# Performance work log

Measured on AMD Instinct MI355X. Metric: run time of the kernel, lower is better.

Reference implementation:

```python
import jax, jax.numpy as jnp
import numpy as np

N_NODES = 50000
N_EDGES = 800000
F_IN = 256
HEADS = 8
OUT_CH = 10  # hard-coded in the source GATv2Conv(in, 10, heads=H)
HIDDEN = HEADS * OUT_CH  # 80
NEG_SLOPE = 0.2  # PyG GATv2Conv default


def _gatv2_layer(x, src, dst, Wl, Wr, att, b, n):
    """One GATv2Conv layer (eval mode, concat=True, self-loops already added).
    x: [n, F_in]; src/dst: [E_tot] int; Wl/Wr: [F_in, H*C]; att: [H, C]; b: [H*C].
    """
    xl = (x @ Wl).reshape(n, HEADS, OUT_CH)  # source-side transform
    xr = (x @ Wr).reshape(n, HEADS, OUT_CH)  # target-side transform
    # gather -> LeakyReLU -> attention logit per edge/head
    e = jax.nn.leaky_relu(xl[src] + xr[dst], NEG_SLOPE)      # [E, H, C]
    logits = jnp.einsum('ehc,hc->eh', e, att)                # [E, H]
    # segment softmax over incoming edges of each target node
    m = jax.ops.segment_max(logits, dst, num_segments=n)     # [n, H]
    ex = jnp.exp(logits - m[dst])
    denom = jax.ops.segment_sum(ex, dst, num_segments=n)     # [n, H]
    alpha = ex / (denom[dst] + 1e-16)                        # [E, H]
    # scatter-add aggregation of weighted source messages
    out = jax.ops.segment_sum(xl[src] * alpha[:, :, None], dst, num_segments=n)
    return out.reshape(n, HIDDEN) + b


def _gat_forward(x, edge_index, params):
    n = x.shape[0]
    loops = jnp.arange(n, dtype=edge_index.dtype)
    src = jnp.concatenate([edge_index[0], loops])  # add self loops (PyG default)
    dst = jnp.concatenate([edge_index[1], loops])
    for (Wl, Wr, att, b) in params:
        x = jax.nn.elu(_gatv2_layer(x, src, dst, Wl, Wr, att, b, n))
    return x


def setup_inputs() -> dict:
    key = jax.random.key(0)
    ks = jax.random.split(key, 16)
    x = jax.random.normal(ks[0], (N_NODES, F_IN), dtype=jnp.float32)
    edge_index = jax.random.randint(ks[1], (2, N_EDGES), 0, N_NODES, dtype=jnp.int64)
    inp = {'x': x, 'edge_index': edge_index}
    dims_in = [F_IN, HIDDEN, HIDDEN]
    for i, d_in in enumerate(dims_in):
        k0, k1, k2 = jax.random.split(ks[2 + i], 3)
        s = 1.0 / np.sqrt(d_in)
        inp[f'Wl{i}'] = jax.random.normal(k0, (d_in, HIDDEN), dtype=jnp.float32) * s
        inp[f'Wr{i}'] = jax.random.normal(k1, (d_in, HIDDEN), dtype=jnp.float32) * s
        inp[f'att{i}'] = jax.random.normal(k2, (HEADS, OUT_CH), dtype=jnp.float32) * 0.1
        inp[f'b{i}'] = jnp.zeros((HIDDEN,), dtype=jnp.float32)
    return inp


def reference(x, edge_index, Wl0, Wr0, att0, b0, Wl1, Wr1, att1, b1, Wl2, Wr2, att2, b2):
    params = [(Wl0, Wr0, att0, b0), (Wl1, Wr1, att1, b1), (Wl2, Wr2, att2, b2)]
    return _gat_forward(x, edge_index, params)
```

## Files before the change

kernel.cpp:

```cpp
#include <hip/hip_runtime.h>
#include <math.h>

#define N_NODES 50000
#define N_EDGES 800000
#define E_TOT   (N_EDGES + N_NODES)
#define HEADS   8
#define OUTC    10
#define HID     80
#define NEG_SLOPE 0.2f


__global__ __launch_bounds__(256) void hist_k(const int* __restrict__ ei, int* __restrict__ cnt) {
    int e = blockIdx.x * blockDim.x + threadIdx.x;
    if (e >= E_TOT) return;
    int d = (e < N_EDGES) ? ei[N_EDGES + e] : (e - N_EDGES);
    atomicAdd(&cnt[d], 1);
}

__global__ __launch_bounds__(1024) void scan_k(const int* __restrict__ cnt, int* __restrict__ rowptr) {
    __shared__ int wsum[16];
    __shared__ int carry_s;
    const int tid = threadIdx.x;
    const int lane = tid & 63, wid = tid >> 6;
    if (tid == 0) carry_s = 0;
    __syncthreads();
    for (int base = 0; base < N_NODES; base += 1024) {
        int i = base + tid;
        int v = (i < N_NODES) ? cnt[i] : 0;
        int s = v;
        #pragma unroll
        for (int off = 1; off < 64; off <<= 1) {
            int t = __shfl_up(s, off, 64);
            if (lane >= off) s += t;
        }
        if (lane == 63) wsum[wid] = s;
        int carry = carry_s;
        __syncthreads();
        if (wid == 0 && lane < 16) {
            int w = wsum[lane];
            #pragma unroll
            for (int off = 1; off < 16; off <<= 1) {
                int t = __shfl_up(w, off, 16);
                if (lane >= off) w += t;
            }
            wsum[lane] = w;
        }
        __syncthreads();
        int woff = (wid > 0) ? wsum[wid - 1] : 0;
        int incl = s + woff;
        int excl = incl - v;
        if (i < N_NODES) rowptr[i] = carry + excl;
        int total = wsum[15];
        __syncthreads();
        if (tid == 0) carry_s = carry + total;
        __syncthreads();
    }
    if (tid == 0) rowptr[N_NODES] = carry_s;
}

__global__ __launch_bounds__(256) void scatter_k(const int* __restrict__ ei,
                                                 const int* __restrict__ rowptr,
                                                 int* __restrict__ cursor,
                                                 int* __restrict__ csr) {
    int e = blockIdx.x * blockDim.x + threadIdx.x;
    if (e >= E_TOT) return;
    int s, d;
    if (e < N_EDGES) { s = ei[e]; d = ei[N_EDGES + e]; }
    else { s = e - N_EDGES; d = s; }
    int pos = rowptr[d] + atomicAdd(&cursor[d], 1);
    csr[pos] = s;
}


__global__ __launch_bounds__(256) void gemm3_k(const float* __restrict__ A, int K,
                                               const float* __restrict__ Wl,
                                               const float* __restrict__ Wr,
                                               float* __restrict__ xl,
                                               float* __restrict__ xr) {
    __shared__ float4 sa[64][4];
    const int tid = threadIdx.x;
    const int lane = tid & 63;
    const int wv = __builtin_amdgcn_readfirstlane(tid >> 6);
    const int mat = wv >> 1;
    const int j0 = (wv & 1) * 40;
    const int row0 = blockIdx.x * 64;
    const int row = row0 + lane;

    const float* __restrict__ W = mat ? Wr : Wl;
    float* __restrict__ Xo = mat ? xr : xl;

    const int lr = tid >> 2;
    const int lq = tid & 3;
    const int lrow = (row0 + lr < N_NODES) ? (row0 + lr) : (N_NODES - 1);
    const float* __restrict__ Asrc = A + (size_t)lrow * K + lq * 4;

    float acc[40];
    #pragma unroll
    for (int j = 0; j < 40; ++j) acc[j] = 0.f;

    for (int kb = 0; kb < K; kb += 16) {
        sa[lr][lq] = *reinterpret_cast<const float4*>(Asrc + kb);
        __syncthreads();

        float4 ar[4];
        #pragma unroll
        for (int q = 0; q < 4; ++q) ar[q] = sa[lane][q];

        #pragma unroll
        for (int q = 0; q < 4; ++q) {
            #pragma unroll
            for (int t = 0; t < 4; ++t) {
                const float av = (t == 0) ? ar[q].x : (t == 1) ? ar[q].y
                               : (t == 2) ? ar[q].z : ar[q].w;
                const float* __restrict__ wrow = W + (size_t)(kb + q * 4 + t) * HID + j0;
                #pragma unroll
                for (int c4 = 0; c4 < 10; ++c4) {
                    const float4 w = *reinterpret_cast<const float4*>(wrow + c4 * 4);
                    acc[c4 * 4 + 0] = fmaf(av, w.x, acc[c4 * 4 + 0]);
                    acc[c4 * 4 + 1] = fmaf(av, w.y, acc[c4 * 4 + 1]);
                    acc[c4 * 4 + 2] = fmaf(av, w.z, acc[c4 * 4 + 2]);
                    acc[c4 * 4 + 3] = fmaf(av, w.w, acc[c4 * 4 + 3]);
                }
            }
        }
        __syncthreads();
    }

    if (row < N_NODES) {
        float* op = Xo + (size_t)row * HID + j0;
        #pragma unroll
        for (int c4 = 0; c4 < 10; ++c4)
            *reinterpret_cast<float4*>(op + c4 * 4) =
                make_float4(acc[c4 * 4 + 0], acc[c4 * 4 + 1], acc[c4 * 4 + 2], acc[c4 * 4 + 3]);
    }
}


__global__ __launch_bounds__(256) void agg2_k(const float* __restrict__ xl,
                                              const float* __restrict__ xr,
                                              const int* __restrict__ rowptr,
                                              const int* __restrict__ csr,
                                              const float* __restrict__ att,
                                              const float* __restrict__ bias,
                                              float* __restrict__ out) {
    const int tid = threadIdx.x;
    const int lane = tid & 63;
    const int node = blockIdx.x * 4 + (tid >> 6);
    if (node >= N_NODES) return;
    const int eg = lane >> 3;
    const int h = lane & 7;
    const int cb = h * 10;

    float att10[10], xr10[10];
    #pragma unroll
    for (int c = 0; c < 10; ++c) {
        att10[c] = att[cb + c];
        xr10[c] = xr[(size_t)node * HID + cb + c];
    }
    const int ro = rowptr[node];
    const int deg = rowptr[node + 1] - ro;

    float m = -INFINITY, s = 0.f;
    float acc[10];
    #pragma unroll
    for (int c = 0; c < 10; ++c) acc[c] = 0.f;

    for (int i = eg; i < deg; i += 8) {
        const int src = csr[ro + i];
        const float* xlp = xl + (size_t)src * HID + cb;
        float xl10[10];
        float logit = 0.f;
        #pragma unroll
        for (int c = 0; c < 10; ++c) {
            xl10[c] = xlp[c];
            float e = xl10[c] + xr10[c];
            e = (e > 0.f) ? e : NEG_SLOPE * e;
            logit = fmaf(e, att10[c], logit);
        }
        const float nm = fmaxf(m, logit);
        const float scale = __expf(m - nm);
        const float p = __expf(logit - nm);
        s = s * scale + p;
        #pragma unroll
        for (int c = 0; c < 10; ++c) acc[c] = acc[c] * scale + p * xl10[c];
        m = nm;
    }

    #pragma unroll
    for (int off = 8; off <= 32; off <<= 1) {
        const float om = __shfl_xor(m, off, 64);
        const float os = __shfl_xor(s, off, 64);
        float oacc[10];
        #pragma unroll
        for (int c = 0; c < 10; ++c) oacc[c] = __shfl_xor(acc[c], off, 64);
        const float nm = fmaxf(m, om);
        const float sc1 = (m == -INFINITY) ? 0.f : __expf(m - nm);
        const float sc2 = (om == -INFINITY) ? 0.f : __expf(om - nm);
        s = s * sc1 + os * sc2;
        #pragma unroll
        for (int c = 0; c < 10; ++c) acc[c] = acc[c] * sc1 + oacc[c] * sc2;
        m = nm;
    }

    if (lane < 8) {
        const float inv = 1.f / (s + 1e-16f);
        #pragma unroll
        for (int c = 0; c < 10; ++c) {
            float v = acc[c] * inv + bias[cb + c];
            v = (v > 0.f) ? v : (__expf(v) - 1.f);
            out[(size_t)node * HID + cb + c] = v;
        }
    }
}


extern "C" void kernel_launch(void* const* d_in, const int* in_sizes, int n_in,
                              void* d_out, int out_size, void* d_ws, size_t ws_size,
                              hipStream_t stream) {
    const float* x  = (const float*)d_in[0];
    const int*   ei = (const int*)d_in[1];
    const float* Wl[3]   = {(const float*)d_in[2], (const float*)d_in[6],  (const float*)d_in[10]};
    const float* Wr[3]   = {(const float*)d_in[3], (const float*)d_in[7],  (const float*)d_in[11]};
    const float* attp[3] = {(const float*)d_in[4], (const float*)d_in[8],  (const float*)d_in[12]};
    const float* bp[3]   = {(const float*)d_in[5], (const float*)d_in[9],  (const float*)d_in[13]};

    char* ws = (char*)d_ws;
    size_t off = 0;
    auto alloc = [&](size_t bytes) -> void* {
        void* p = ws + off;
        off += (bytes + 255) & ~(size_t)255;
        return p;
    };
    int* cnt    = (int*)alloc((size_t)N_NODES * 4);
    int* cursor = (int*)alloc((size_t)N_NODES * 4);
    int* rowptr = (int*)alloc((size_t)(N_NODES + 1) * 4);
    int* csr    = (int*)alloc((size_t)E_TOT * 4);
    float* xl   = (float*)alloc((size_t)N_NODES * HID * 4);
    float* xr   = (float*)alloc((size_t)N_NODES * HID * 4);
    float* actA = (float*)alloc((size_t)N_NODES * HID * 4);
    float* actB = (float*)alloc((size_t)N_NODES * HID * 4);

    hipMemsetAsync(cnt, 0, (size_t)N_NODES * 4, stream);
    hipMemsetAsync(cursor, 0, (size_t)N_NODES * 4, stream);

    hist_k<<<(E_TOT + 255) / 256, 256, 0, stream>>>(ei, cnt);
    scan_k<<<1, 1024, 0, stream>>>(cnt, rowptr);
    scatter_k<<<(E_TOT + 255) / 256, 256, 0, stream>>>(ei, rowptr, cursor, csr);

    for (int l = 0; l < 3; ++l) {
        const float* act_in = (l == 0) ? x : (l == 1 ? actA : actB);
        const int K = (l == 0) ? 256 : 80;
        gemm3_k<<<(N_NODES + 63) / 64, 256, 0, stream>>>(act_in, K, Wl[l], Wr[l], xl, xr);
        float* out_l = (l == 0) ? actA : (l == 1 ? actB : (float*)d_out);
        agg2_k<<<N_NODES / 4, 256, 0, stream>>>(xl, xr, rowptr, csr, attp[l], bp[l], out_l);
    }
}
```

Before: 557.2 us.

## Use transposed activation layout so GEMM reads coalesced columns without LDS

Adds a tiled transpose of the input features and makes the aggregation kernel write its activations in feature-major (transposed) layout for the next layer. The new GEMM kernel reads two adjacent rows per lane directly from global memory, with no shared-memory staging or barriers. Each wave computes 20 output columns, and a grid dimension selects Wl or Wr. The aim is to remove LDS syncs and raise per-thread reuse. In exchange it adds an extra transpose pass, and the transposed stores from aggregation are strided and poorly coalesced.

```diff
diff --git a/kernel.cpp b/kernel.cpp
--- a/kernel.cpp
+++ b/kernel.cpp
@@ -4,6 +4,7 @@
 #define N_NODES 50000
 #define N_EDGES 800000
 #define E_TOT   (N_EDGES + N_NODES)
+#define F_IN    256
 #define HEADS   8
 #define OUTC    10
 #define HID     80
@@ -72,66 +73,86 @@
 }
 
 
-__global__ __launch_bounds__(256) void gemm3_k(const float* __restrict__ A, int K,
+__global__ __launch_bounds__(256) void transp_k(const float* __restrict__ in,
+                                                float* __restrict__ outT) {
+    __shared__ float t[64][65];
+    const int tx = threadIdx.x & 63;
+    const int ty = threadIdx.x >> 6;
+    const int r0 = blockIdx.x * 64;
+    const int c0 = blockIdx.y * 64;
+    #pragma unroll
+    for (int i = 0; i < 16; ++i) {
+        int r = ty * 16 + i;
+        int gr = r0 + r;
+        if (gr < N_NODES) t[r][tx] = in[(size_t)gr * F_IN + c0 + tx];
+    }
+    __syncthreads();
+    #pragma unroll
+    for (int i = 0; i < 16; ++i) {
+        int c = ty * 16 + i;
+        int gr = r0 + tx;
+        if (gr < N_NODES) outT[(size_t)(c0 + c) * N_NODES + gr] = t[tx][c];
+    }
+}
+
+
+__global__ __launch_bounds__(256) void gemm4_k(const float* __restrict__ AT, int K,
                                                const float* __restrict__ Wl,
                                                const float* __restrict__ Wr,
                                                float* __restrict__ xl,
                                                float* __restrict__ xr) {
-    __shared__ float4 sa[64][4];
-    const int tid = threadIdx.x;
-    const int lane = tid & 63;
-    const int wv = __builtin_amdgcn_readfirstlane(tid >> 6);
-    const int mat = wv >> 1;
-    const int j0 = (wv & 1) * 40;
-    const int row0 = blockIdx.x * 64;
-    const int row = row0 + lane;
+    const int lane = threadIdx.x & 63;
+    const int wv = __builtin_amdgcn_readfirstlane(threadIdx.x >> 6);
+    const int mat = blockIdx.y;
+    const int j0 = wv * 20;
+    const int row0 = blockIdx.x * 128;
+    const int rbase = row0 + 2 * lane;
+    const int rload = (rbase <= N_NODES - 2) ? rbase : (N_NODES - 2);
 
     const float* __restrict__ W = mat ? Wr : Wl;
     float* __restrict__ Xo = mat ? xr : xl;
 
-    const int lr = tid >> 2;
-    const int lq = tid & 3;
-    const int lrow = (row0 + lr < N_NODES) ? (row0 + lr) : (N_NODES - 1);
-    const float* __restrict__ Asrc = A + (size_t)lrow * K + lq * 4;
-
-    float acc[40];
-    #pragma unroll
-    for (int j = 0; j < 40; ++j) acc[j] = 0.f;
-
-    for (int kb = 0; kb < K; kb += 16) {
-        sa[lr][lq] = *reinterpret_cast<const float4*>(Asrc + kb);
-        __syncthreads();
-
-        float4 ar[4];
-        #pragma unroll
-        for (int q = 0; q < 4; ++q) ar[q] = sa[lane][q];
-
-        #pragma unroll
-        for (int q = 0; q < 4; ++q) {
+    float acc0[20], acc1[20];
+    #pragma unroll
+    for (int j = 0; j < 20; ++j) { acc0[j] = 0.f; acc1[j] = 0.f; }
+
+    for (int kb = 0; kb < K; kb += 4) {
+        float2 a[4];
+        #pragma unroll
+        for (int t = 0; t < 4; ++t)
+            a[t] = *reinterpret_cast<const float2*>(AT + (size_t)(kb + t) * N_NODES + rload);
+        #pragma unroll
+        for (int t = 0; t < 4; ++t) {
+            const float* __restrict__ wrow = W + (size_t)(kb + t) * HID + j0;
+            const float ax = a[t].x, ay = a[t].y;
             #pragma unroll
-            for (int t = 0; t < 4; ++t) {
-                const float av = (t == 0) ? ar[q].x : (t == 1) ? ar[q].y
-                               : (t == 2) ? ar[q].z : ar[q].w;
-                const float* __restrict__ wrow = W + (size_t)(kb + q * 4 + t) * HID + j0;
-                #pragma unroll
-                for (int c4 = 0; c4 < 10; ++c4) {
-                    const float4 w = *reinterpret_cast<const float4*>(wrow + c4 * 4);
-                    acc[c4 * 4 + 0] = fmaf(av, w.x, acc[c4 * 4 + 0]);
-                    acc[c4 * 4 + 1] = fmaf(av, w.y, acc[c4 * 4 + 1]);
-                    acc[c4 * 4 + 2] = fmaf(av, w.z, acc[c4 * 4 + 2]);
-                    acc[c4 * 4 + 3] = fmaf(av, w.w, acc[c4 * 4 + 3]);
-                }
+            for (int q = 0; q < 5; ++q) {
+                const float4 w = *reinterpret_cast<const float4*>(wrow + q * 4);
+                acc0[q * 4 + 0] = fmaf(ax, w.x, acc0[q * 4 + 0]);
+                acc0[q * 4 + 1] = fmaf(ax, w.y, acc0[q * 4 + 1]);
+                acc0[q * 4 + 2] = fmaf(ax, w.z, acc0[q * 4 + 2]);
+                acc0[q * 4 + 3] = fmaf(ax, w.w, acc0[q * 4 + 3]);
+                acc1[q * 4 + 0] = fmaf(ay, w.x, acc1[q * 4 + 0]);
+                acc1[q * 4 + 1] = fmaf(ay, w.y, acc1[q * 4 + 1]);
+                acc1[q * 4 + 2] = fmaf(ay, w.z, acc1[q * 4 + 2]);
+                acc1[q * 4 + 3] = fmaf(ay, w.w, acc1[q * 4 + 3]);
             }
         }
-        __syncthreads();
-    }
-
-    if (row < N_NODES) {
-        float* op = Xo + (size_t)row * HID + j0;
-        #pragma unroll
-        for (int c4 = 0; c4 < 10; ++c4)
-            *reinterpret_cast<float4*>(op + c4 * 4) =
-                make_float4(acc[c4 * 4 + 0], acc[c4 * 4 + 1], acc[c4 * 4 + 2], acc[c4 * 4 + 3]);
+    }
+
+    if (rbase < N_NODES) {
+        float* op = Xo + (size_t)rbase * HID + j0;
+        #pragma unroll
+        for (int q = 0; q < 5; ++q)
+            *reinterpret_cast<float4*>(op + q * 4) =
+                make_float4(acc0[q * 4 + 0], acc0[q * 4 + 1], acc0[q * 4 + 2], acc0[q * 4 + 3]);
+    }
+    if (rbase + 1 < N_NODES) {
+        float* op = Xo + (size_t)(rbase + 1) * HID + j0;
+        #pragma unroll
+        for (int q = 0; q < 5; ++q)
+            *reinterpret_cast<float4*>(op + q * 4) =
+                make_float4(acc1[q * 4 + 0], acc1[q * 4 + 1], acc1[q * 4 + 2], acc1[q * 4 + 3]);
     }
 }
 
@@ -142,7 +163,8 @@
                                               const int* __restrict__ csr,
                                               const float* __restrict__ att,
                                               const float* __restrict__ bias,
-                                              float* __restrict__ out) {
+                                              float* __restrict__ out,
+                                              float* __restrict__ outT) {
     const int tid = threadIdx.x;
     const int lane = tid & 63;
     const int node = blockIdx.x * 4 + (tid >> 6);
@@ -208,7 +230,8 @@
         for (int c = 0; c < 10; ++c) {
             float v = acc[c] * inv + bias[cb + c];
             v = (v > 0.f) ? v : (__expf(v) - 1.f);
-            out[(size_t)node * HID + cb + c] = v;
+            if (outT) outT[(size_t)(cb + c) * N_NODES + node] = v;
+            else      out[(size_t)node * HID + cb + c] = v;
         }
     }
 }
@@ -237,8 +260,9 @@
     int* csr    = (int*)alloc((size_t)E_TOT * 4);
     float* xl   = (float*)alloc((size_t)N_NODES * HID * 4);
     float* xr   = (float*)alloc((size_t)N_NODES * HID * 4);
-    float* actA = (float*)alloc((size_t)N_NODES * HID * 4);
-    float* actB = (float*)alloc((size_t)N_NODES * HID * 4);
+    float* xT   = (float*)alloc((size_t)F_IN * N_NODES * 4);
+    float* actAT = xT;
+    float* actBT = xT + (size_t)HID * N_NODES;
 
     hipMemsetAsync(cnt, 0, (size_t)N_NODES * 4, stream);
     hipMemsetAsync(cursor, 0, (size_t)N_NODES * 4, stream);
@@ -247,11 +271,16 @@
     scan_k<<<1, 1024, 0, stream>>>(cnt, rowptr);
     scatter_k<<<(E_TOT + 255) / 256, 256, 0, stream>>>(ei, rowptr, cursor, csr);
 
+    transp_k<<<dim3(782, 4), 256, 0, stream>>>(x, xT);
+
+    const float* AT_l[3] = {xT, actAT, actBT};
+    float* outT_l[3]     = {actAT, actBT, nullptr};
     for (int l = 0; l < 3; ++l) {
-        const float* act_in = (l == 0) ? x : (l == 1 ? actA : actB);
-        const int K = (l == 0) ? 256 : 80;
-        gemm3_k<<<(N_NODES + 63) / 64, 256, 0, stream>>>(act_in, K, Wl[l], Wr[l], xl, xr);
-        float* out_l = (l == 0) ? actA : (l == 1 ? actB : (float*)d_out);
-        agg2_k<<<N_NODES / 4, 256, 0, stream>>>(xl, xr, rowptr, csr, attp[l], bp[l], out_l);
-    }
-}
+        const int K = (l == 0) ? F_IN : HID;
+        gemm4_k<<<dim3((N_NODES + 127) / 128, 2), 256, 0, stream>>>(
+            AT_l[l], K, Wl[l], Wr[l], xl, xr);
+        float* out_l = (l == 2) ? (float*)d_out : nullptr;
+        agg2_k<<<N_NODES / 4, 256, 0, stream>>>(xl, xr, rowptr, csr, attp[l], bp[l],
+                                                out_l, outT_l[l]);
+    }
+}
```

Result: slower. 610.3 us (+9.5%).

## Retile node-feature GEMM to 128-row blocks with two rows per thread

Applied to the files above, without the earlier changes.

The dual-weight GEMM is restructured so each block handles 128 rows for one weight matrix, chosen by blockIdx.y. Each wave owns 20 output columns and each thread computes two rows, so every weight float4 load feeds two rows of FMAs. The A tile is stored transposed in shared memory as 16x128 floats. This is meant to halve weight-load traffic per FMA and improve register reuse, at the cost of more blocks and some shared-memory bank conflicts on the transposed stores.

```diff
diff --git a/kernel.cpp b/kernel.cpp
--- a/kernel.cpp
+++ b/kernel.cpp
@@ -4,6 +4,7 @@
 #define N_NODES 50000
 #define N_EDGES 800000
 #define E_TOT   (N_EDGES + N_NODES)
+#define F_IN    256
 #define HEADS   8
 #define OUTC    10
 #define HID     80
@@ -72,66 +73,78 @@
 }
 
 
-__global__ __launch_bounds__(256) void gemm3_k(const float* __restrict__ A, int K,
+__global__ __launch_bounds__(256) void gemm5_k(const float* __restrict__ A, int K,
                                                const float* __restrict__ Wl,
                                                const float* __restrict__ Wr,
                                                float* __restrict__ xl,
                                                float* __restrict__ xr) {
-    __shared__ float4 sa[64][4];
+    __shared__ float sa[16][128];
     const int tid = threadIdx.x;
     const int lane = tid & 63;
     const int wv = __builtin_amdgcn_readfirstlane(tid >> 6);
-    const int mat = wv >> 1;
-    const int j0 = (wv & 1) * 40;
-    const int row0 = blockIdx.x * 64;
-    const int row = row0 + lane;
+    const int mat = blockIdx.y;
+    const int j0 = wv * 20;
+    const int row0 = blockIdx.x * 128;
 
     const float* __restrict__ W = mat ? Wr : Wl;
     float* __restrict__ Xo = mat ? xr : xl;
 
-    const int lr = tid >> 2;
-    const int lq = tid & 3;
-    const int lrow = (row0 + lr < N_NODES) ? (row0 + lr) : (N_NODES - 1);
-    const float* __restrict__ Asrc = A + (size_t)lrow * K + lq * 4;
-
-    float acc[40];
-    #pragma unroll
-    for (int j = 0; j < 40; ++j) acc[j] = 0.f;
+    const int sr = tid >> 2;
+    const int sq = tid & 3;
+
+    float acc0[20], acc1[20];
+    #pragma unroll
+    for (int j = 0; j < 20; ++j) { acc0[j] = 0.f; acc1[j] = 0.f; }
 
     for (int kb = 0; kb < K; kb += 16) {
-        sa[lr][lq] = *reinterpret_cast<const float4*>(Asrc + kb);
-        __syncthreads();
-
-        float4 ar[4];
-        #pragma unroll
-        for (int q = 0; q < 4; ++q) ar[q] = sa[lane][q];
-
-        #pragma unroll
-        for (int q = 0; q < 4; ++q) {
+        #pragma unroll
+        for (int h = 0; h < 2; ++h) {
+            const int gr = row0 + h * 64 + sr;
+            const int grc = (gr < N_NODES) ? gr : (N_NODES - 1);
+            const float4 v = *reinterpret_cast<const float4*>(
+                A + (size_t)grc * K + kb + sq * 4);
+            sa[sq * 4 + 0][h * 64 + sr] = v.x;
+            sa[sq * 4 + 1][h * 64 + sr] = v.y;
+            sa[sq * 4 + 2][h * 64 + sr] = v.z;
+            sa[sq * 4 + 3][h * 64 + sr] = v.w;
+        }
+        __syncthreads();
+        #pragma unroll
+        for (int k = 0; k < 16; ++k) {
+            const float a0 = sa[k][lane];
+            const float a1 = sa[k][64 + lane];
+            const float* __restrict__ wrow = W + (size_t)(kb + k) * HID + j0;
             #pragma unroll
-            for (int t = 0; t < 4; ++t) {
-                const float av = (t == 0) ? ar[q].x : (t == 1) ? ar[q].y
-                               : (t == 2) ? ar[q].z : ar[q].w;
-                const float* __restrict__ wrow = W + (size_t)(kb + q * 4 + t) * HID + j0;
-                #pragma unroll
-                for (int c4 = 0; c4 < 10; ++c4) {
-                    const float4 w = *reinterpret_cast<const float4*>(wrow + c4 * 4);
-                    acc[c4 * 4 + 0] = fmaf(av, w.x, acc[c4 * 4 + 0]);
-                    acc[c4 * 4 + 1] = fmaf(av, w.y, acc[c4 * 4 + 1]);
-                    acc[c4 * 4 + 2] = fmaf(av, w.z, acc[c4 * 4 + 2]);
-                    acc[c4 * 4 + 3] = fmaf(av, w.w, acc[c4 * 4 + 3]);
-                }
+            for (int q = 0; q < 5; ++q) {
+                const float4 w = *reinterpret_cast<const float4*>(wrow + q * 4);
+                acc0[q * 4 + 0] = fmaf(a0, w.x, acc0[q * 4 + 0]);
+                acc0[q * 4 + 1] = fmaf(a0, w.y, acc0[q * 4 + 1]);
+                acc0[q * 4 + 2] = fmaf(a0, w.z, acc0[q * 4 + 2]);
+                acc0[q * 4 + 3] = fmaf(a0, w.w, acc0[q * 4 + 3]);
+                acc1[q * 4 + 0] = fmaf(a1, w.x, acc1[q * 4 + 0]);
+                acc1[q * 4 + 1] = fmaf(a1, w.y, acc1[q * 4 + 1]);
+                acc1[q * 4 + 2] = fmaf(a1, w.z, acc1[q * 4 + 2]);
+                acc1[q * 4 + 3] = fmaf(a1, w.w, acc1[q * 4 + 3]);
             }
         }
         __syncthreads();
     }
 
-    if (row < N_NODES) {
-        float* op = Xo + (size_t)row * HID + j0;
-        #pragma unroll
-        for (int c4 = 0; c4 < 10; ++c4)
-            *reinterpret_cast<float4*>(op + c4 * 4) =
-                make_float4(acc[c4 * 4 + 0], acc[c4 * 4 + 1], acc[c4 * 4 + 2], acc[c4 * 4 + 3]);
+    const int r0 = row0 + lane;
+    if (r0 < N_NODES) {
+        float* op = Xo + (size_t)r0 * HID + j0;
+        #pragma unroll
+        for (int q = 0; q < 5; ++q)
+            *reinterpret_cast<float4*>(op + q * 4) =
+                make_float4(acc0[q * 4 + 0], acc0[q * 4 + 1], acc0[q * 4 + 2], acc0[q * 4 + 3]);
+    }
+    const int r1 = row0 + 64 + lane;
+    if (r1 < N_NODES) {
+        float* op = Xo + (size_t)r1 * HID + j0;
+        #pragma unroll
+        for (int q = 0; q < 5; ++q)
+            *reinterpret_cast<float4*>(op + q * 4) =
+                make_float4(acc1[q * 4 + 0], acc1[q * 4 + 1], acc1[q * 4 + 2], acc1[q * 4 + 3]);
     }
 }
 
@@ -249,8 +262,9 @@
 
     for (int l = 0; l < 3; ++l) {
         const float* act_in = (l == 0) ? x : (l == 1 ? actA : actB);
-        const int K = (l == 0) ? 256 : 80;
-        gemm3_k<<<(N_NODES + 63) / 64, 256, 0, stream>>>(act_in, K, Wl[l], Wr[l], xl, xr);
+        const int K = (l == 0) ? F_IN : HID;
+        gemm5_k<<<dim3((N_NODES + 127) / 128, 2), 256, 0, stream>>>(
+            act_in, K, Wl[l], Wr[l], xl, xr);
         float* out_l = (l == 0) ? actA : (l == 1 ? actB : (float*)d_out);
         agg2_k<<<N_NODES / 4, 256, 0, stream>>>(xl, xr, rowptr, csr, attp[l], bp[l], out_l);
     }
```

After: 514.6 us. 7.6% less time.

## Replace FP32 FMA GEMM with split-bf16 MFMA GEMM and bf16 activation outputs

Applied to the files above, without the earlier changes.

The scalar FP32 node-feature GEMM is replaced by an MFMA bf16 16x16x32 kernel that emulates FP32 accuracy with a hi/lo split (three MFMAs per tile). The input features and weights are converted to hi/lo bf16 buffers, with K padded to 96 for the hidden layers, and the aggregation kernel writes hi/lo bf16 activations directly for the next layer's GEMM. This moves the dense transform onto the matrix cores, in exchange for extra conversion kernels, memsets, and a small loss of precision. The B operands are read straight from global memory with no LDS staging.

```diff
diff --git a/kernel.cpp b/kernel.cpp
--- a/kernel.cpp
+++ b/kernel.cpp
@@ -4,10 +4,23 @@
 #define N_NODES 50000
 #define N_EDGES 800000
 #define E_TOT   (N_EDGES + N_NODES)
+#define F_IN    256
 #define HEADS   8
 #define OUTC    10
 #define HID     80
 #define NEG_SLOPE 0.2f
+
+typedef __attribute__((ext_vector_type(8))) short bfrag;
+typedef __attribute__((ext_vector_type(4))) float ffrag;
+
+__device__ __forceinline__ unsigned short f2bf(float f) {
+    unsigned u = __float_as_uint(f);
+    u += 0x7FFFu + ((u >> 16) & 1u);
+    return (unsigned short)(u >> 16);
+}
+__device__ __forceinline__ float bf2f(unsigned short h) {
+    return __uint_as_float((unsigned)h << 16);
+}
 
 
 __global__ __launch_bounds__(256) void hist_k(const int* __restrict__ ei, int* __restrict__ cnt) {
@@ -72,66 +85,89 @@
 }
 
 
-__global__ __launch_bounds__(256) void gemm3_k(const float* __restrict__ A, int K,
-                                               const float* __restrict__ Wl,
+__global__ __launch_bounds__(256) void convA_k(const float* __restrict__ in,
+                                               unsigned short* __restrict__ hi,
+                                               unsigned short* __restrict__ lo,
+                                               int n, int K, int Kp) {
+    const int cpr = Kp >> 2;
+    const size_t total = (size_t)n * cpr;
+    for (size_t c = (size_t)blockIdx.x * blockDim.x + threadIdx.x; c < total;
+         c += (size_t)gridDim.x * blockDim.x) {
+        const int row = (int)(c / cpr);
+        const int k = (int)(c % cpr) << 2;
+        float4 v = make_float4(0.f, 0.f, 0.f, 0.f);
+        if (k < K) v = *reinterpret_cast<const float4*>(in + (size_t)row * K + k);
+        unsigned short h0 = f2bf(v.x), h1 = f2bf(v.y), h2 = f2bf(v.z), h3 = f2bf(v.w);
+        unsigned short l0 = f2bf(v.x - bf2f(h0)), l1 = f2bf(v.y - bf2f(h1));
+        unsigned short l2 = f2bf(v.z - bf2f(h2)), l3 = f2bf(v.w - bf2f(h3));
+        uint2 hp = make_uint2(((unsigned)h1 << 16) | h0, ((unsigned)h3 << 16) | h2);
+        uint2 lp = make_uint2(((unsigned)l1 << 16) | l0, ((unsigned)l3 << 16) | l2);
+        *reinterpret_cast<uint2*>(hi + (size_t)row * Kp + k) = hp;
+        *reinterpret_cast<uint2*>(lo + (size_t)row * Kp + k) = lp;
+    }
+}
+
+
+__global__ __launch_bounds__(256) void convW_k(const float* __restrict__ Wl,
                                                const float* __restrict__ Wr,
-                                               float* __restrict__ xl,
-                                               float* __restrict__ xr) {
-    __shared__ float4 sa[64][4];
-    const int tid = threadIdx.x;
-    const int lane = tid & 63;
-    const int wv = __builtin_amdgcn_readfirstlane(tid >> 6);
-    const int mat = wv >> 1;
-    const int j0 = (wv & 1) * 40;
-    const int row0 = blockIdx.x * 64;
-    const int row = row0 + lane;
-
-    const float* __restrict__ W = mat ? Wr : Wl;
+                                               unsigned short* __restrict__ WTh,
+                                               unsigned short* __restrict__ WTl,
+                                               int K, int Kp) {
+    const int total = 160 * Kp;
+    for (int idx = blockIdx.x * blockDim.x + threadIdx.x; idx < total;
+         idx += gridDim.x * blockDim.x) {
+        const int j = idx / Kp, k = idx % Kp;
+        float v = 0.f;
+        if (k < K) v = (j < 80) ? Wl[(size_t)k * HID + j] : Wr[(size_t)k * HID + (j - 80)];
+        const unsigned short h = f2bf(v);
+        WTh[idx] = h;
+        WTl[idx] = f2bf(v - bf2f(h));
+    }
+}
+
+
+__global__ __launch_bounds__(256) void gemm6_k(
+    const unsigned short* __restrict__ Ahi, const unsigned short* __restrict__ Alo, int Kp,
+    const unsigned short* __restrict__ WTh, const unsigned short* __restrict__ WTl,
+    float* __restrict__ xl, float* __restrict__ xr) {
+    const int lane = threadIdx.x & 63;
+    const int wv = threadIdx.x >> 6;
+    const int mat = blockIdx.y;
+    const int rowbase = blockIdx.x * 64 + wv * 16;
+    const int m = lane & 15, kg = lane >> 4;
+    const int arow = min(rowbase + m, N_NODES - 1);
+
+    const unsigned short* __restrict__ pah = Ahi + (size_t)arow * Kp + kg * 8;
+    const unsigned short* __restrict__ pal = Alo + (size_t)arow * Kp + kg * 8;
+    const unsigned short* __restrict__ pbh = WTh + (size_t)(mat * 80 + m) * Kp + kg * 8;
+    const unsigned short* __restrict__ pbl = WTl + (size_t)(mat * 80 + m) * Kp + kg * 8;
+
+    ffrag acc[5];
+    #pragma unroll
+    for (int ct = 0; ct < 5; ++ct) acc[ct] = (ffrag){0.f, 0.f, 0.f, 0.f};
+
+    for (int kb = 0; kb < Kp; kb += 32) {
+        const bfrag ah = *reinterpret_cast<const bfrag*>(pah + kb);
+        const bfrag al = *reinterpret_cast<const bfrag*>(pal + kb);
+        #pragma unroll
+        for (int ct = 0; ct < 5; ++ct) {
+            const size_t bo = (size_t)ct * 16 * Kp + kb;
+            const bfrag bh = *reinterpret_cast<const bfrag*>(pbh + bo);
+            const bfrag bl = *reinterpret_cast<const bfrag*>(pbl + bo);
+            acc[ct] = __builtin_amdgcn_mfma_f32_16x16x32_bf16(ah, bh, acc[ct], 0, 0, 0);
+            acc[ct] = __builtin_amdgcn_mfma_f32_16x16x32_bf16(ah, bl, acc[ct], 0, 0, 0);
+            acc[ct] = __builtin_amdgcn_mfma_f32_16x16x32_bf16(al, bh, acc[ct], 0, 0, 0);
+        }
+    }
+
     float* __restrict__ Xo = mat ? xr : xl;
-
-    const int lr = tid >> 2;
-    const int lq = tid & 3;
-    const int lrow = (row0 + lr < N_NODES) ? (row0 + lr) : (N_NODES - 1);
-    const float* __restrict__ Asrc = A + (size_t)lrow * K + lq * 4;
-
-    float acc[40];
-    #pragma unroll
-    for (int j = 0; j < 40; ++j) acc[j] = 0.f;
-
-    for (int kb = 0; kb < K; kb += 16) {
-        sa[lr][lq] = *reinterpret_cast<const float4*>(Asrc + kb);
-        __syncthreads();
-
-        float4 ar[4];
-        #pragma unroll
-        for (int q = 0; q < 4; ++q) ar[q] = sa[lane][q];
-
-        #pragma unroll
-        for (int q = 0; q < 4; ++q) {
-            #pragma unroll
-            for (int t = 0; t < 4; ++t) {
-                const float av = (t == 0) ? ar[q].x : (t == 1) ? ar[q].y
-                               : (t == 2) ? ar[q].z : ar[q].w;
-                const float* __restrict__ wrow = W + (size_t)(kb + q * 4 + t) * HID + j0;
-                #pragma unroll
-                for (int c4 = 0; c4 < 10; ++c4) {
-                    const float4 w = *reinterpret_cast<const float4*>(wrow + c4 * 4);
-                    acc[c4 * 4 + 0] = fmaf(av, w.x, acc[c4 * 4 + 0]);
-                    acc[c4 * 4 + 1] = fmaf(av, w.y, acc[c4 * 4 + 1]);
-                    acc[c4 * 4 + 2] = fmaf(av, w.z, acc[c4 * 4 + 2]);
-                    acc[c4 * 4 + 3] = fmaf(av, w.w, acc[c4 * 4 + 3]);
-                }
-            }
-        }
-        __syncthreads();
-    }
-
-    if (row < N_NODES) {
-        float* op = Xo + (size_t)row * HID + j0;
-        #pragma unroll
-        for (int c4 = 0; c4 < 10; ++c4)
-            *reinterpret_cast<float4*>(op + c4 * 4) =
-                make_float4(acc[c4 * 4 + 0], acc[c4 * 4 + 1], acc[c4 * 4 + 2], acc[c4 * 4 + 3]);
+    #pragma unroll
+    for (int ct = 0; ct < 5; ++ct) {
+        #pragma unroll
+        for (int r = 0; r < 4; ++r) {
+            const int row = rowbase + kg * 4 + r;
+            if (row < N_NODES) Xo[(size_t)row * HID + ct * 16 + m] = acc[ct][r];
+        }
     }
 }
 
@@ -142,7 +178,9 @@
                                               const int* __restrict__ csr,
                                               const float* __restrict__ att,
                                               const float* __restrict__ bias,
-                                              float* __restrict__ out) {
+                                              float* __restrict__ outf,
+                                              unsigned short* __restrict__ outh,
+                                              unsigned short* __restrict__ outl) {
     const int tid = threadIdx.x;
     const int lane = tid & 63;
     const int node = blockIdx.x * 4 + (tid >> 6);
@@ -208,7 +246,13 @@
         for (int c = 0; c < 10; ++c) {
             float v = acc[c] * inv + bias[cb + c];
             v = (v > 0.f) ? v : (__expf(v) - 1.f);
-            out[(size_t)node * HID + cb + c] = v;
+            if (outf) {
+                outf[(size_t)node * HID + cb + c] = v;
+            } else {
+                const unsigned short hh = f2bf(v);
+                outh[(size_t)node * 96 + cb + c] = hh;
+                outl[(size_t)node * 96 + cb + c] = f2bf(v - bf2f(hh));
+            }
         }
     }
 }
@@ -237,8 +281,12 @@
     int* csr    = (int*)alloc((size_t)E_TOT * 4);
     float* xl   = (float*)alloc((size_t)N_NODES * HID * 4);
     float* xr   = (float*)alloc((size_t)N_NODES * HID * 4);
-    float* actA = (float*)alloc((size_t)N_NODES * HID * 4);
-    float* actB = (float*)alloc((size_t)N_NODES * HID * 4);
+    unsigned short* Ahi0 = (unsigned short*)alloc((size_t)N_NODES * F_IN * 2);
+    unsigned short* Alo0 = (unsigned short*)alloc((size_t)N_NODES * F_IN * 2);
+    unsigned short* WTh  = (unsigned short*)alloc((size_t)160 * F_IN * 2);
+    unsigned short* WTl  = (unsigned short*)alloc((size_t)160 * F_IN * 2);
+    unsigned short* AhiL = Ahi0;
+    unsigned short* AloL = Alo0;
 
     hipMemsetAsync(cnt, 0, (size_t)N_NODES * 4, stream);
     hipMemsetAsync(cursor, 0, (size_t)N_NODES * 4, stream);
@@ -247,11 +295,22 @@
     scan_k<<<1, 1024, 0, stream>>>(cnt, rowptr);
     scatter_k<<<(E_TOT + 255) / 256, 256, 0, stream>>>(ei, rowptr, cursor, csr);
 
+    convA_k<<<4096, 256, 0, stream>>>(x, Ahi0, Alo0, N_NODES, F_IN, F_IN);
+
     for (int l = 0; l < 3; ++l) {
-        const float* act_in = (l == 0) ? x : (l == 1 ? actA : actB);
-        const int K = (l == 0) ? 256 : 80;
-        gemm3_k<<<(N_NODES + 63) / 64, 256, 0, stream>>>(act_in, K, Wl[l], Wr[l], xl, xr);
-        float* out_l = (l == 0) ? actA : (l == 1 ? actB : (float*)d_out);
-        agg2_k<<<N_NODES / 4, 256, 0, stream>>>(xl, xr, rowptr, csr, attp[l], bp[l], out_l);
-    }
-}
+        const int K  = (l == 0) ? F_IN : HID;
+        const int Kp = (l == 0) ? F_IN : 96;
+        convW_k<<<64, 256, 0, stream>>>(Wl[l], Wr[l], WTh, WTl, K, Kp);
+        gemm6_k<<<dim3((N_NODES + 63) / 64, 2), 256, 0, stream>>>(
+            (l == 0) ? Ahi0 : AhiL, (l == 0) ? Alo0 : AloL, Kp, WTh, WTl, xl, xr);
+        if (l == 0) {
+            hipMemsetAsync(AhiL, 0, (size_t)N_NODES * 96 * 2, stream);
+            hipMemsetAsync(AloL, 0, (size_t)N_NODES * 96 * 2, stream);
+        }
+        float* outf = (l == 2) ? (float*)d_out : nullptr;
+        unsigned short* outh = (l < 2) ? AhiL : nullptr;
+        unsigned short* outl = (l < 2) ? AloL : nullptr;
+        agg2_k<<<N_NODES / 4, 256, 0, stream>>>(xl, xr, rowptr, csr, attp[l], bp[l],
+                                                outf, outh, outl);
+    }
+}
```

Measured after the change: 610.0 us. 9.5% more time.
